# Performance work log

Measured on AMD Instinct MI355X. Metric: run time of the kernel, lower is better.

The kernel has to match this reference:

```python
import jax, jax.numpy as jnp
import numpy as np

GAMMA = 0.99
LMBDA = 0.95


def setup_inputs() -> dict:
    key = jax.random.key(0)
    k1, k2, k3, k4 = jax.random.split(key, 4)
    B, T = 4096, 2048
    return {
        "reward": jax.random.normal(k1, (B, T), dtype=jnp.float32),
        "terminated": jax.random.randint(k2, (B, T), 0, 2, dtype=jnp.int32),
        "value": jax.random.normal(k3, (B, T), dtype=jnp.float32),
        "next_value": jax.random.normal(k4, (B, T), dtype=jnp.float32),
    }


def _gae(reward, not_done, value, next_value):
    # All inputs [B, T]. Backward-time scan over T with carry gae [B].
    # delta_t = r_t + gamma * V(s_{t+1}) * nd_t - V(s_t)
    # A_t = delta_t + gamma * lmbda * nd_t * A_{t+1}
    xs = (reward.T, not_done.T, value.T, next_value.T)  # each [T, B]

    def step(gae, x):
        r, nd, v, nv = x
        delta = r + GAMMA * nv * nd - v
        gae = delta + GAMMA * LMBDA * nd * gae
        return gae, gae

    init = jnp.zeros(reward.shape[0], dtype=reward.dtype)
    _, adv_t = jax.lax.scan(step, init, xs, reverse=True)  # [T, B]
    advantages = adv_t.T  # [B, T]
    returns = advantages + value
    return advantages, returns


def reference(reward, terminated, value, next_value):
    not_done = 1.0 - terminated.astype(reward.dtype)
    return _gae(reward, not_done, value, next_value)
```

## Files before the change

kernel.cpp:

```cpp
#include <hip/hip_runtime.h>


constexpr float GAMMA = 0.99f;
constexpr float LMBDA = 0.95f;
constexpr int   T     = 2048;
constexpr int   TPB   = 256;
constexpr int   E     = T / TPB;
constexpr int   NW    = TPB / 64;

__global__ __launch_bounds__(TPB) void gae_kernel(
    const float* __restrict__ reward,
    const int*   __restrict__ term,
    const float* __restrict__ value,
    const float* __restrict__ next_value,
    float* __restrict__ adv_out,
    float* __restrict__ ret_out)
{
    const int j    = threadIdx.x;
    const int wave = j >> 6;
    const int lane = j & 63;
    const size_t base = (size_t)blockIdx.x * T + (size_t)j * E;

    float4 rA = ((const float4*)(reward     + base))[0];
    float4 rB = ((const float4*)(reward     + base))[1];
    int4   tA = ((const int4*  )(term       + base))[0];
    int4   tB = ((const int4*  )(term       + base))[1];
    float4 vA = ((const float4*)(value      + base))[0];
    float4 vB = ((const float4*)(value      + base))[1];
    float4 nA = ((const float4*)(next_value + base))[0];
    float4 nB = ((const float4*)(next_value + base))[1];

    float r [E] = {rA.x, rA.y, rA.z, rA.w, rB.x, rB.y, rB.z, rB.w};
    float nd[E] = {1.f - (float)tA.x, 1.f - (float)tA.y, 1.f - (float)tA.z, 1.f - (float)tA.w,
                   1.f - (float)tB.x, 1.f - (float)tB.y, 1.f - (float)tB.z, 1.f - (float)tB.w};
    float v [E] = {vA.x, vA.y, vA.z, vA.w, vB.x, vB.y, vB.z, vB.w};
    float nv[E] = {nA.x, nA.y, nA.z, nA.w, nB.x, nB.y, nB.z, nB.w};

    float loc[E], P[E];
    {
        float g = 0.f, p = 1.f;
        #pragma unroll
        for (int t = E - 1; t >= 0; --t) {
            float c     = (GAMMA * LMBDA) * nd[t];
            float delta = fmaf(GAMMA * nv[t], nd[t], r[t]) - v[t];
            g = fmaf(c, g, delta);
            p *= c;
            loc[t] = g;
            P[t]   = p;
        }
    }

    float A = loc[0], Bc = P[0];
    #pragma unroll
    for (int off = 1; off < 64; off <<= 1) {
        float a2 = __shfl_down(A,  off, 64);
        float b2 = __shfl_down(Bc, off, 64);
        if (lane + off < 64) {
            A  = fmaf(Bc, a2, A);
            Bc *= b2;
        }
    }

    __shared__ float sA[NW], sB[NW];
    if (lane == 0) { sA[wave] = A; sB[wave] = Bc; }

    float eA = __shfl_down(A,  1, 64);
    float eB = __shfl_down(Bc, 1, 64);
    if (lane == 63) { eA = 0.f; eB = 1.f; }

    __syncthreads();

    float wcarry = 0.f;
    #pragma unroll
    for (int w = NW - 1; w > 0; --w) {
        if (w > wave) wcarry = fmaf(sB[w], wcarry, sA[w]);
    }

    const float gin = fmaf(eB, wcarry, eA);

    float adv[E], ret[E];
    #pragma unroll
    for (int t = 0; t < E; ++t) {
        adv[t] = fmaf(P[t], gin, loc[t]);
        ret[t] = adv[t] + v[t];
    }

    ((float4*)(adv_out + base))[0] = make_float4(adv[0], adv[1], adv[2], adv[3]);
    ((float4*)(adv_out + base))[1] = make_float4(adv[4], adv[5], adv[6], adv[7]);
    ((float4*)(ret_out + base))[0] = make_float4(ret[0], ret[1], ret[2], ret[3]);
    ((float4*)(ret_out + base))[1] = make_float4(ret[4], ret[5], ret[6], ret[7]);
}

extern "C" void kernel_launch(void* const* d_in, const int* in_sizes, int n_in,
                              void* d_out, int out_size, void* d_ws, size_t ws_size,
                              hipStream_t stream) {
    const float* reward     = (const float*)d_in[0];
    const int*   term       = (const int*  )d_in[1];
    const float* value      = (const float*)d_in[2];
    const float* next_value = (const float*)d_in[3];

    const int BT = in_sizes[0];
    const int B  = BT / T;

    float* adv = (float*)d_out;
    float* ret = adv + BT;

    gae_kernel<<<B, TPB, 0, stream>>>(reward, term, value, next_value, adv, ret);
}
```

Measured before the change: 176.8 us.

## Assign one wavefront per row with sequential segment scans and prefetched loads

Each row is now handled by a single 64-lane wavefront that walks four 512-element segments from the end backward. The carry passes between segments through a wave shuffle rather than shared memory, which removes the __syncthreads. The next segment's loads are issued before the current segment is scanned, so memory latency overlaps with compute. In exchange each wave does four dependent segment scans, raising per-wave latency and register pressure from holding two Raw buffers.

```diff
diff --git a/kernel.cpp b/kernel.cpp
--- a/kernel.cpp
+++ b/kernel.cpp
@@ -1,53 +1,56 @@
 #include <hip/hip_runtime.h>
 
 
-constexpr float GAMMA = 0.99f;
-constexpr float LMBDA = 0.95f;
-constexpr int   T     = 2048;
-constexpr int   TPB   = 256;
-constexpr int   E     = T / TPB;
-constexpr int   NW    = TPB / 64;
+constexpr float GAMMA  = 0.99f;
+constexpr float LMBDA  = 0.95f;
+constexpr int   T      = 2048;
+constexpr int   SEGLEN = 512;
+constexpr int   EPT    = SEGLEN / 64;
+constexpr int   WPB    = 4;
 
-__global__ __launch_bounds__(TPB) void gae_kernel(
-    const float* __restrict__ reward,
-    const int*   __restrict__ term,
-    const float* __restrict__ value,
-    const float* __restrict__ next_value,
-    float* __restrict__ adv_out,
-    float* __restrict__ ret_out)
+struct Raw {
+    float4 r0, r1; int4 t0, t1; float4 v0, v1; float4 n0, n1;
+};
+
+__device__ __forceinline__ Raw load_raw(const float* __restrict__ reward,
+                                        const int*   __restrict__ term,
+                                        const float* __restrict__ value,
+                                        const float* __restrict__ next_value,
+                                        size_t o)
 {
-    const int j    = threadIdx.x;
-    const int wave = j >> 6;
-    const int lane = j & 63;
-    const size_t base = (size_t)blockIdx.x * T + (size_t)j * E;
+    Raw x;
+    x.r0 = ((const float4*)(reward     + o))[0];
+    x.r1 = ((const float4*)(reward     + o))[1];
+    x.t0 = ((const int4*  )(term       + o))[0];
+    x.t1 = ((const int4*  )(term       + o))[1];
+    x.v0 = ((const float4*)(value      + o))[0];
+    x.v1 = ((const float4*)(value      + o))[1];
+    x.n0 = ((const float4*)(next_value + o))[0];
+    x.n1 = ((const float4*)(next_value + o))[1];
+    return x;
+}
 
-    float4 rA = ((const float4*)(reward     + base))[0];
-    float4 rB = ((const float4*)(reward     + base))[1];
-    int4   tA = ((const int4*  )(term       + base))[0];
-    int4   tB = ((const int4*  )(term       + base))[1];
-    float4 vA = ((const float4*)(value      + base))[0];
-    float4 vB = ((const float4*)(value      + base))[1];
-    float4 nA = ((const float4*)(next_value + base))[0];
-    float4 nB = ((const float4*)(next_value + base))[1];
+__device__ __forceinline__ float seg_scan_store(const Raw& x, int lane, float g,
+                                                float* __restrict__ adv_out,
+                                                float* __restrict__ ret_out,
+                                                size_t o)
+{
+    float r [EPT] = {x.r0.x, x.r0.y, x.r0.z, x.r0.w, x.r1.x, x.r1.y, x.r1.z, x.r1.w};
+    float nd[EPT] = {1.f - (float)x.t0.x, 1.f - (float)x.t0.y, 1.f - (float)x.t0.z, 1.f - (float)x.t0.w,
+                     1.f - (float)x.t1.x, 1.f - (float)x.t1.y, 1.f - (float)x.t1.z, 1.f - (float)x.t1.w};
+    float vv[EPT] = {x.v0.x, x.v0.y, x.v0.z, x.v0.w, x.v1.x, x.v1.y, x.v1.z, x.v1.w};
+    float nv[EPT] = {x.n0.x, x.n0.y, x.n0.z, x.n0.w, x.n1.x, x.n1.y, x.n1.z, x.n1.w};
 
-    float r [E] = {rA.x, rA.y, rA.z, rA.w, rB.x, rB.y, rB.z, rB.w};
-    float nd[E] = {1.f - (float)tA.x, 1.f - (float)tA.y, 1.f - (float)tA.z, 1.f - (float)tA.w,
-                   1.f - (float)tB.x, 1.f - (float)tB.y, 1.f - (float)tB.z, 1.f - (float)tB.w};
-    float v [E] = {vA.x, vA.y, vA.z, vA.w, vB.x, vB.y, vB.z, vB.w};
-    float nv[E] = {nA.x, nA.y, nA.z, nA.w, nB.x, nB.y, nB.z, nB.w};
-
-    float loc[E], P[E];
-    {
-        float g = 0.f, p = 1.f;
-        #pragma unroll
-        for (int t = E - 1; t >= 0; --t) {
-            float c     = (GAMMA * LMBDA) * nd[t];
-            float delta = fmaf(GAMMA * nv[t], nd[t], r[t]) - v[t];
-            g = fmaf(c, g, delta);
-            p *= c;
-            loc[t] = g;
-            P[t]   = p;
-        }
+    float loc[EPT], P[EPT];
+    float gg = 0.f, p = 1.f;
+    #pragma unroll
+    for (int t = EPT - 1; t >= 0; --t) {
+        float c     = (GAMMA * LMBDA) * nd[t];
+        float delta = fmaf(GAMMA * nv[t], nd[t], r[t]) - vv[t];
+        gg = fmaf(c, gg, delta);
+        p *= c;
+        loc[t] = gg;
+        P[t]   = p;
     }
 
     float A = loc[0], Bc = P[0];
@@ -61,34 +64,56 @@
         }
     }
 
-    __shared__ float sA[NW], sB[NW];
-    if (lane == 0) { sA[wave] = A; sB[wave] = Bc; }
-
     float eA = __shfl_down(A,  1, 64);
     float eB = __shfl_down(Bc, 1, 64);
     if (lane == 63) { eA = 0.f; eB = 1.f; }
 
-    __syncthreads();
+    const float gout = __shfl(fmaf(Bc, g, A), 0, 64);
 
-    float wcarry = 0.f;
-    #pragma unroll
-    for (int w = NW - 1; w > 0; --w) {
-        if (w > wave) wcarry = fmaf(sB[w], wcarry, sA[w]);
-    }
+    const float gin = fmaf(eB, g, eA);
 
-    const float gin = fmaf(eB, wcarry, eA);
+    float a0 = fmaf(P[0], gin, loc[0]), a1 = fmaf(P[1], gin, loc[1]);
+    float a2 = fmaf(P[2], gin, loc[2]), a3 = fmaf(P[3], gin, loc[3]);
+    float a4 = fmaf(P[4], gin, loc[4]), a5 = fmaf(P[5], gin, loc[5]);
+    float a6 = fmaf(P[6], gin, loc[6]), a7 = fmaf(P[7], gin, loc[7]);
 
-    float adv[E], ret[E];
-    #pragma unroll
-    for (int t = 0; t < E; ++t) {
-        adv[t] = fmaf(P[t], gin, loc[t]);
-        ret[t] = adv[t] + v[t];
-    }
+    ((float4*)(adv_out + o))[0] = make_float4(a0, a1, a2, a3);
+    ((float4*)(adv_out + o))[1] = make_float4(a4, a5, a6, a7);
+    ((float4*)(ret_out + o))[0] = make_float4(a0 + vv[0], a1 + vv[1], a2 + vv[2], a3 + vv[3]);
+    ((float4*)(ret_out + o))[1] = make_float4(a4 + vv[4], a5 + vv[5], a6 + vv[6], a7 + vv[7]);
 
-    ((float4*)(adv_out + base))[0] = make_float4(adv[0], adv[1], adv[2], adv[3]);
-    ((float4*)(adv_out + base))[1] = make_float4(adv[4], adv[5], adv[6], adv[7]);
-    ((float4*)(ret_out + base))[0] = make_float4(ret[0], ret[1], ret[2], ret[3]);
-    ((float4*)(ret_out + base))[1] = make_float4(ret[4], ret[5], ret[6], ret[7]);
+    return gout;
+}
+
+__global__ __launch_bounds__(256) void gae_kernel(
+    const float* __restrict__ reward,
+    const int*   __restrict__ term,
+    const float* __restrict__ value,
+    const float* __restrict__ next_value,
+    float* __restrict__ adv_out,
+    float* __restrict__ ret_out,
+    int B)
+{
+    const int wave = threadIdx.x >> 6;
+    const int lane = threadIdx.x & 63;
+    const int row  = blockIdx.x * WPB + wave;
+    if (row >= B) return;
+
+    const size_t rowbase = (size_t)row * T + (size_t)lane * EPT;
+    const size_t o3 = rowbase + 3 * SEGLEN;
+    const size_t o2 = rowbase + 2 * SEGLEN;
+    const size_t o1 = rowbase + 1 * SEGLEN;
+    const size_t o0 = rowbase;
+
+    Raw x3 = load_raw(reward, term, value, next_value, o3);
+    Raw x2 = load_raw(reward, term, value, next_value, o2);
+    float g = 0.f;
+    g = seg_scan_store(x3, lane, g, adv_out, ret_out, o3);
+    Raw x1 = load_raw(reward, term, value, next_value, o1);
+    g = seg_scan_store(x2, lane, g, adv_out, ret_out, o2);
+    Raw x0 = load_raw(reward, term, value, next_value, o0);
+    g = seg_scan_store(x1, lane, g, adv_out, ret_out, o1);
+    (void)seg_scan_store(x0, lane, g, adv_out, ret_out, o0);
 }
 
 extern "C" void kernel_launch(void* const* d_in, const int* in_sizes, int n_in,
@@ -105,5 +130,7 @@
     float* adv = (float*)d_out;
     float* ret = adv + BT;
 
-    gae_kernel<<<B, TPB, 0, stream>>>(reward, term, value, next_value, adv, ret);
+    const int grid = (B + WPB - 1) / WPB;
+    gae_kernel<<<grid, 64 * WPB, 0, stream>>>(
+        reward, term, value, next_value, adv, ret, B);
 }
```

New measurement: 192.7 us. +9.0%, slower.
